# Performance work log

Hardware: AMD Instinct MI355X
Metric: run time of the kernel (lower is better)

Reference implementation:

```python
import jax, jax.numpy as jnp
import numpy as np

T_STEPS = 10          # hardcoded T_pos = T_neg = 10 in the source
SCALE = 0.125         # hardcoded attention scale
N_HEADS, N_KV_HEADS, HEAD_DIM = 32, 8, 128
DIM, HIDDEN = 4096, 14336
EPS = 1e-5

def _spike(x):
    # IFNode Heaviside fire (forward only; spikes are exact 0/1)
    return (x >= 0.0).astype(x.dtype)

def if_node(x_seq):
    """spikingjelly IFNode, step_mode='m': v += x; fire at v>=1; hard reset to 0."""
    def step(v, xt):
        v = v + xt
        s = _spike(v - 1.0)
        v = v * (1.0 - s)
        return v, s
    _, spikes = jax.lax.scan(step, jnp.zeros_like(x_seq[0]), x_seq)
    return spikes  # [T, ...]

def if_proj(x2d, W):
    # linear proj of constant-over-time input, then IF spiking over T steps
    y = x2d @ W.T                                   # [N, dout]
    return if_node(jnp.broadcast_to(y[None], (T_STEPS,) + y.shape))  # [T, N, dout]

def rmsnorm(x, w):
    return x * jax.lax.rsqrt(jnp.mean(x * x, axis=-1, keepdims=True) + EPS) * w

def attention(x, wq, wk, wv, wo):
    N, C = x.shape
    xp, xn = jax.nn.relu(x), jax.nn.relu(-x)
    xq = if_proj(xp, wq) - if_proj(xn, wq)          # [T, N, H*D]
    xk = if_proj(xp, wk) - if_proj(xn, wk)          # [T, N, Hkv*D]
    xv = if_proj(xp, wv) - if_proj(xn, wv)
    rep = N_HEADS // N_KV_HEADS
    xq = xq.reshape(T_STEPS, N, N_HEADS, HEAD_DIM)
    # repeat_interleave along token dim + view == tile over kv-head axis
    xk = jnp.tile(xk.reshape(T_STEPS, N, N_KV_HEADS, HEAD_DIM), (1, 1, rep, 1))
    xv = jnp.tile(xv.reshape(T_STEPS, N, N_KV_HEADS, HEAD_DIM), (1, 1, rep, 1))
    # NOTE: source computes per-token head-mixing scores [T,N,H,H], not token attention
    attn = jnp.einsum('tnid,tnjd->tnij', xq, xk) * SCALE
    xa = jnp.einsum('tnij,tnjd->tnid', attn, xv)    # [T,N,H,D]
    xa = jnp.swapaxes(xa, -1, -2).reshape(T_STEPS, N, C)  # transpose(-1,-2).reshape
    return (xa @ wo.T).mean(0)

def ffn(x, w1, w2, w3):
    xp, xn = jax.nn.relu(x), jax.nn.relu(-x)
    x_w3 = if_proj(xp, w3) - if_proj(xn, w3)        # [T, N, hidden]
    x_w1p = if_proj(xp, w1)                          # only positive branch for w1
    return (x_w1p.mean(0) * x_w3.mean(0)) @ w2.T

def setup_inputs() -> dict:
    ks = jax.random.split(jax.random.key(0), 9)
    std = 0.02
    return {
        'x': jax.random.normal(ks[0], (256, DIM), jnp.float32),
        'freqs_cis': jnp.zeros((256, HEAD_DIM // 2), jnp.float32),
        'attn_norm_w': jnp.ones((DIM,), jnp.float32),
        'ffn_norm_w': jnp.ones((DIM,), jnp.float32),
        'wq': std * jax.random.normal(ks[1], (N_HEADS * HEAD_DIM, DIM), jnp.float32),
        'wk': std * jax.random.normal(ks[2], (N_KV_HEADS * HEAD_DIM, DIM), jnp.float32),
        'wv': std * jax.random.normal(ks[3], (N_KV_HEADS * HEAD_DIM, DIM), jnp.float32),
        'wo': std * jax.random.normal(ks[4], (DIM, N_HEADS * HEAD_DIM), jnp.float32),
        'w1': std * jax.random.normal(ks[5], (HIDDEN, DIM), jnp.float32),
        'w2': std * jax.random.normal(ks[6], (DIM, HIDDEN), jnp.float32),
        'w3': std * jax.random.normal(ks[7], (HIDDEN, DIM), jnp.float32),
    }

def reference(x, freqs_cis, attn_norm_w, ffn_norm_w, wq, wk, wv, wo, w1, w2, w3):
    h = x + attention(rmsnorm(x, attn_norm_w), wq, wk, wv, wo)
    out = h + ffn(rmsnorm(h, ffn_norm_w), w1, w2, w3)
    return out
```

## Files before the change

### kernel.cpp

```cpp
#include <hip/hip_runtime.h>
#include <math.h>


typedef double f64x4 __attribute__((ext_vector_type(4)));

__device__ __forceinline__ unsigned spike_pat_d(double y) {
    double v = 0.0; unsigned p = 0u;
#pragma unroll
    for (int t = 0; t < 10; ++t) {
        v += y;
        bool s = (v >= 1.0);
        p |= s ? (1u << t) : 0u;
        v = s ? 0.0 : v;
    }
    return p;
}

__device__ __forceinline__ int spike_count_d(double y) {
    double v = 0.0; int c = 0;
#pragma unroll
    for (int t = 0; t < 10; ++t) {
        v += y;
        bool s = (v >= 1.0);
        c += s ? 1 : 0;
        v = s ? 0.0 : v;
    }
    return c;
}

__global__ __launch_bounds__(256) void rms_f_kernel(const float* __restrict__ x,
                                                    const float* __restrict__ w,
                                                    double* __restrict__ out)
{
    const int row = blockIdx.x, tid = threadIdx.x;
    const float4* xr = (const float4*)(x + (size_t)row * 4096);
    const float4* wr = (const float4*)w;
    double* orow = out + (size_t)row * 4096;
    float4 v[4];
    double ss = 0.0;
#pragma unroll
    for (int i = 0; i < 4; ++i) {
        v[i] = xr[tid + (i << 8)];
        ss += (double)v[i].x * v[i].x + (double)v[i].y * v[i].y +
              (double)v[i].z * v[i].z + (double)v[i].w * v[i].w;
    }
#pragma unroll
    for (int off = 32; off > 0; off >>= 1) ss += __shfl_down(ss, off, 64);
    __shared__ double red[4];
    if ((tid & 63) == 0) red[tid >> 6] = ss;
    __syncthreads();
    double m = (red[0] + red[1] + red[2] + red[3]) * (1.0 / 4096.0);
    double sc = 1.0 / sqrt(m + 1e-5);
#pragma unroll
    for (int i = 0; i < 4; ++i) {
        float4 wv = wr[tid + (i << 8)];
        int b = (tid + (i << 8)) << 2;
        orow[b + 0] = ((double)v[i].x * sc) * (double)wv.x;
        orow[b + 1] = ((double)v[i].y * sc) * (double)wv.y;
        orow[b + 2] = ((double)v[i].z * sc) * (double)wv.z;
        orow[b + 3] = ((double)v[i].w * sc) * (double)wv.w;
    }
}

__global__ __launch_bounds__(256) void rms_d_kernel(const double* __restrict__ x,
                                                    const float* __restrict__ w,
                                                    double* __restrict__ out)
{
    const int row = blockIdx.x, tid = threadIdx.x;
    const double2* xr = (const double2*)(x + (size_t)row * 4096);
    const float2* wr = (const float2*)w;
    double* orow = out + (size_t)row * 4096;
    double2 v[8];
    double ss = 0.0;
#pragma unroll
    for (int i = 0; i < 8; ++i) {
        v[i] = xr[tid + (i << 8)];
        ss += v[i].x * v[i].x + v[i].y * v[i].y;
    }
#pragma unroll
    for (int off = 32; off > 0; off >>= 1) ss += __shfl_down(ss, off, 64);
    __shared__ double red[4];
    if ((tid & 63) == 0) red[tid >> 6] = ss;
    __syncthreads();
    double m = (red[0] + red[1] + red[2] + red[3]) * (1.0 / 4096.0);
    double sc = 1.0 / sqrt(m + 1e-5);
#pragma unroll
    for (int i = 0; i < 8; ++i) {
        float2 wv = wr[tid + (i << 8)];
        int b = (tid + (i << 8)) << 1;
        orow[b + 0] = (v[i].x * sc) * (double)wv.x;
        orow[b + 1] = (v[i].y * sc) * (double)wv.y;
    }
}

template <int MODE, int WT>
__global__ __launch_bounds__(256, 2) void gemm_kernel(
    const void* __restrict__ Av, const void* __restrict__ A2v,
    const float* __restrict__ W, const void* __restrict__ ADDv,
    void* __restrict__ C0v, int K, int N)
{
    constexpr bool DUAL = (MODE == 0 || MODE == 1);
    constexpr int NB = DUAL ? 2 : 1;
    constexpr int BMN = 32 * WT;
    constexpr int EPT = 2 * WT;
    __shared__ __align__(16) double As[NB][16][BMN + 4];
    __shared__ __align__(16) float  Ws[16][BMN + 8];

    const int tid = threadIdx.x;
    const int m0 = blockIdx.y * BMN, n0 = blockIdx.x * BMN;

    const int lrow = tid / (16 / EPT);
    const int lk   = (tid % (16 / EPT)) * EPT;

    const int l  = tid & 63;
    const int wid = tid >> 6;
    const int wm = wid >> 1, wn = wid & 1;
    const int lr = l & 15;
    const int kf = l >> 4;

    f64x4 accp[WT][WT] = {};
    f64x4 accn[WT][WT] = {};

    const float* Wpt = W + (size_t)(n0 + lrow) * K + lk;
    const double* Apt = nullptr;
    const unsigned char* S1t = nullptr;
    const signed char* S3t = nullptr;
    if constexpr (MODE <= 3) {
        Apt = (const double*)Av + (size_t)(m0 + lrow) * K + lk;
    } else {
        S1t = (const unsigned char*)Av + (size_t)(m0 + lrow) * K + lk;
        S3t = (const signed char*)A2v + (size_t)(m0 + lrow) * K + lk;
    }

    auto LOAD = [&](int k0, double* a, float* w) {
        if constexpr (MODE == 4) {
            uchar4 c1 = *(const uchar4*)(S1t + k0);
            char4  c3 = *(const char4*)(S3t + k0);
            a[0] = ((double)c1.x * 0.1) * ((double)c3.x * 0.1);
            a[1] = ((double)c1.y * 0.1) * ((double)c3.y * 0.1);
            a[2] = ((double)c1.z * 0.1) * ((double)c3.z * 0.1);
            a[3] = ((double)c1.w * 0.1) * ((double)c3.w * 0.1);
        } else if constexpr (EPT == 4) {
            double2 a01 = *(const double2*)(Apt + k0);
            double2 a23 = *(const double2*)(Apt + k0 + 2);
            a[0] = a01.x; a[1] = a01.y; a[2] = a23.x; a[3] = a23.y;
        } else {
            double2 a01 = *(const double2*)(Apt + k0);
            a[0] = a01.x; a[1] = a01.y;
        }
        if constexpr (EPT == 4) {
            float4 wv = *(const float4*)(Wpt + k0);
            w[0] = wv.x; w[1] = wv.y; w[2] = wv.z; w[3] = wv.w;
        } else {
            float2 wv = *(const float2*)(Wpt + k0);
            w[0] = wv.x; w[1] = wv.y;
        }
    };

    double a_cur[EPT]; float w_cur[EPT];
    LOAD(0, a_cur, w_cur);

    for (int k0 = 0; k0 < K; k0 += 16) {
#pragma unroll
        for (int j = 0; j < EPT; ++j) {
            if constexpr (DUAL) {
                As[0][lk + j][lrow] = fmax(a_cur[j], 0.0);
                As[1][lk + j][lrow] = fmax(-a_cur[j], 0.0);
            } else if constexpr (MODE == 2) {
                As[0][lk + j][lrow] = fmax(a_cur[j], 0.0);
            } else {
                As[0][lk + j][lrow] = a_cur[j];
            }
            Ws[lk + j][lrow] = w_cur[j];
        }
        __syncthreads();

        double a_nxt[EPT]; float w_nxt[EPT];
        if (k0 + 16 < K) LOAD(k0 + 16, a_nxt, w_nxt);

#pragma unroll
        for (int ks = 0; ks < 4; ++ks) {
            const int kk = (ks << 2) + kf;
            double b[WT], p[WT];
#pragma unroll
            for (int nt = 0; nt < WT; ++nt)
                b[nt] = (double)Ws[kk][wn * (16 * WT) + nt * 16 + lr];
#pragma unroll
            for (int mt = 0; mt < WT; ++mt)
                p[mt] = As[0][kk][wm * (16 * WT) + mt * 16 + lr];
#pragma unroll
            for (int mt = 0; mt < WT; ++mt)
#pragma unroll
                for (int nt = 0; nt < WT; ++nt)
                    accp[mt][nt] = __builtin_amdgcn_mfma_f64_16x16x4f64(
                        p[mt], b[nt], accp[mt][nt], 0, 0, 0);
            if constexpr (DUAL) {
                double q[WT];
#pragma unroll
                for (int mt = 0; mt < WT; ++mt)
                    q[mt] = As[1][kk][wm * (16 * WT) + mt * 16 + lr];
#pragma unroll
                for (int mt = 0; mt < WT; ++mt)
#pragma unroll
                    for (int nt = 0; nt < WT; ++nt)
                        accn[mt][nt] = __builtin_amdgcn_mfma_f64_16x16x4f64(
                            q[mt], b[nt], accn[mt][nt], 0, 0, 0);
            }
        }
        __syncthreads();

#pragma unroll
        for (int j = 0; j < EPT; ++j) a_cur[j] = a_nxt[j];
#pragma unroll
        for (int j = 0; j < EPT; ++j) w_cur[j] = w_nxt[j];
    }

#pragma unroll
    for (int mt = 0; mt < WT; ++mt) {
#pragma unroll
        for (int nt = 0; nt < WT; ++nt) {
#pragma unroll
            for (int r = 0; r < 4; ++r) {
                const int m = m0 + wm * (16 * WT) + mt * 16 + (kf << 2) + r;
                const int n = n0 + wn * (16 * WT) + nt * 16 + lr;
                const size_t idx = (size_t)m * N + n;
                const double vp = accp[mt][nt][r];
                if constexpr (MODE == 0) {
                    const double vn = accn[mt][nt][r];
                    ((unsigned*)C0v)[idx] =
                        spike_pat_d(vp) | (spike_pat_d(vn) << 16);
                } else if constexpr (MODE == 1) {
                    const double vn = accn[mt][nt][r];
                    ((signed char*)C0v)[idx] =
                        (signed char)(spike_count_d(vp) - spike_count_d(vn));
                } else if constexpr (MODE == 2) {
                    ((unsigned char*)C0v)[idx] =
                        (unsigned char)spike_count_d(vp);
                } else if constexpr (MODE == 3) {
                    ((double*)C0v)[idx] =
                        (double)((const float*)ADDv)[idx] + vp;
                } else {
                    ((float*)C0v)[idx] =
                        (float)(((const double*)ADDv)[idx] + vp);
                }
            }
        }
    }
}

__global__ __launch_bounds__(256) void attn_kernel(
    const unsigned* __restrict__ patq_g, const unsigned* __restrict__ patk_g,
    const unsigned* __restrict__ patv_g, double* __restrict__ Aout)
{
    __shared__ __align__(16) unsigned patq[4096];
    __shared__ __align__(16) unsigned patk[1024];
    __shared__ __align__(16) unsigned patv[1024];
    __shared__ int S8[10][32][8];
    const int n = blockIdx.x, tid = threadIdx.x;

    const uint4* q4 = (const uint4*)(patq_g + (size_t)n * 4096);
#pragma unroll
    for (int r = 0; r < 4; ++r)
        ((uint4*)patq)[tid + (r << 8)] = q4[tid + (r << 8)];
    ((uint4*)patk)[tid] = ((const uint4*)(patk_g + (size_t)n * 1024))[tid];
    ((uint4*)patv)[tid] = ((const uint4*)(patv_g + (size_t)n * 1024))[tid];
    __syncthreads();

    const int hi = tid >> 3;
    const int j8 = tid & 7;

    int sacc[10] = {0, 0, 0, 0, 0, 0, 0, 0, 0, 0};
    for (int d = 0; d < 128; ++d) {
        unsigned q = patq[(hi << 7) + d];
        unsigned k = patk[(j8 << 7) + d];
        unsigned qp = q & 0xFFFFu, qn = q >> 16;
        unsigned kp = k & 0xFFFFu, kn = k >> 16;
        unsigned pos = (qp & kp) | (qn & kn);
        unsigned neg = (qp & kn) | (qn & kp);
#pragma unroll
        for (int t = 0; t < 10; ++t)
            sacc[t] += (int)((pos >> t) & 1u) - (int)((neg >> t) & 1u);
    }
#pragma unroll
    for (int t = 0; t < 10; ++t) S8[t][hi][j8] = sacc[t];
    __syncthreads();

    float xacc[16];
#pragma unroll
    for (int dd = 0; dd < 16; ++dd) xacc[dd] = 0.f;

    for (int t = 0; t < 10; ++t) {
        int s8r[8];
#pragma unroll
        for (int jj = 0; jj < 8; ++jj) s8r[jj] = S8[t][hi][jj];
#pragma unroll
        for (int dd = 0; dd < 16; ++dd) {
            int d = (j8 << 4) + dd;
            int acc = 0;
#pragma unroll
            for (int jj = 0; jj < 8; ++jj) {
                unsigned v = patv[(jj << 7) + d];
                int vv = (int)((v >> t) & 1u) - (int)((v >> (t + 16)) & 1u);
                acc += s8r[jj] * vv;
            }
            xacc[dd] += 0.5f * (float)acc;
        }
    }
#pragma unroll
    for (int dd = 0; dd < 16; ++dd) {
        int d = (j8 << 4) + dd;
        Aout[(size_t)n * 4096 + (d << 5) + hi] = (double)xacc[dd] / 10.0;
    }
}

extern "C" void kernel_launch(void* const* d_in, const int* in_sizes, int n_in,
                              void* d_out, int out_size, void* d_ws, size_t ws_size,
                              hipStream_t stream)
{
    const float* x   = (const float*)d_in[0];
    const float* anw = (const float*)d_in[2];
    const float* fnw = (const float*)d_in[3];
    const float* wq  = (const float*)d_in[4];
    const float* wk  = (const float*)d_in[5];
    const float* wv  = (const float*)d_in[6];
    const float* wo  = (const float*)d_in[7];
    const float* w1  = (const float*)d_in[8];
    const float* w2  = (const float*)d_in[9];
    const float* w3  = (const float*)d_in[10];
    float* out = (float*)d_out;

    double* h1 = (double*)d_ws;
    double* Ap = h1 + 1048576;
    double* hb = Ap + 1048576;
    double* h2 = hb + 1048576;
    unsigned* patq = (unsigned*)(h2 + 1048576);
    unsigned* patk = patq + 1048576;
    unsigned* patv = patk + 262144;
    unsigned char* s1 = (unsigned char*)(patv + 262144);
    signed char*  s3 = (signed char*)(s1 + 3670016);

    dim3 blk(256);
    rms_f_kernel<<<dim3(256), blk, 0, stream>>>(x, anw, h1);
    gemm_kernel<0, 2><<<dim3(64, 4), blk, 0, stream>>>(h1, nullptr, wq, nullptr, patq, 4096, 4096);
    gemm_kernel<0, 1><<<dim3(32, 8), blk, 0, stream>>>(h1, nullptr, wk, nullptr, patk, 4096, 1024);
    gemm_kernel<0, 1><<<dim3(32, 8), blk, 0, stream>>>(h1, nullptr, wv, nullptr, patv, 4096, 1024);
    attn_kernel<<<dim3(256), blk, 0, stream>>>(patq, patk, patv, Ap);
    gemm_kernel<3, 2><<<dim3(64, 4), blk, 0, stream>>>(Ap, nullptr, wo, x, hb, 4096, 4096);
    rms_d_kernel<<<dim3(256), blk, 0, stream>>>(hb, fnw, h2);
    gemm_kernel<1, 2><<<dim3(224, 4), blk, 0, stream>>>(h2, nullptr, w3, nullptr, s3, 4096, 14336);
    gemm_kernel<2, 2><<<dim3(224, 4), blk, 0, stream>>>(h2, nullptr, w1, nullptr, s1, 4096, 14336);
    gemm_kernel<4, 2><<<dim3(64, 4), blk, 0, stream>>>(s1, s3, w2, hb, out, 14336, 4096);
}
```

Baseline: 4.347 ms.

## Double-buffer GEMM shared tiles, fuse QKV and FFN13 launches, derive negative branch algebraically

The GEMM body now keeps two shared-memory buffers, so the next K-slice is stored while the current one is consumed, leaving one barrier per iteration instead of two. The dual relu(x)/relu(-x) path stores the raw activation once, applies fmax when reading it, and recovers the negative product as relu(x)·W − x·W. This removes the second As buffer and its extra stores. The Q/K/V GEMMs become one launch, as do the w3/w1 FFN GEMMs, which cuts launch count and fills the GPU better. The risk is that the subtraction changes f64 rounding slightly, which could flip spike thresholds right at the boundary.

After: 3.910 ms. -10.1%, faster.

```diff
diff --git a/kernel.cpp b/kernel.cpp
--- a/kernel.cpp
+++ b/kernel.cpp
@@ -93,33 +93,27 @@
     }
 }
 
-template <int MODE, int WT>
-__global__ __launch_bounds__(256, 2) void gemm_kernel(
+template <int MODE>
+__device__ __forceinline__ void gemm_body(
     const void* __restrict__ Av, const void* __restrict__ A2v,
     const float* __restrict__ W, const void* __restrict__ ADDv,
-    void* __restrict__ C0v, int K, int N)
+    void* __restrict__ C0v, int K, int N, int m0, int n0,
+    double As[2][16][68], float Ws[2][16][72])
 {
     constexpr bool DUAL = (MODE == 0 || MODE == 1);
-    constexpr int NB = DUAL ? 2 : 1;
-    constexpr int BMN = 32 * WT;
-    constexpr int EPT = 2 * WT;
-    __shared__ __align__(16) double As[NB][16][BMN + 4];
-    __shared__ __align__(16) float  Ws[16][BMN + 8];
-
     const int tid = threadIdx.x;
-    const int m0 = blockIdx.y * BMN, n0 = blockIdx.x * BMN;
-
-    const int lrow = tid / (16 / EPT);
-    const int lk   = (tid % (16 / EPT)) * EPT;
-
-    const int l  = tid & 63;
+
+    const int lrow = tid >> 2;
+    const int lk   = (tid & 3) << 2;
+
+    const int l   = tid & 63;
     const int wid = tid >> 6;
     const int wm = wid >> 1, wn = wid & 1;
     const int lr = l & 15;
     const int kf = l >> 4;
 
-    f64x4 accp[WT][WT] = {};
-    f64x4 accn[WT][WT] = {};
+    f64x4 accA[2][2] = {};
+    f64x4 accR[2][2] = {};
 
     const float* Wpt = W + (size_t)(n0 + lrow) * K + lk;
     const double* Apt = nullptr;
@@ -140,112 +134,145 @@
             a[1] = ((double)c1.y * 0.1) * ((double)c3.y * 0.1);
             a[2] = ((double)c1.z * 0.1) * ((double)c3.z * 0.1);
             a[3] = ((double)c1.w * 0.1) * ((double)c3.w * 0.1);
-        } else if constexpr (EPT == 4) {
+        } else {
             double2 a01 = *(const double2*)(Apt + k0);
             double2 a23 = *(const double2*)(Apt + k0 + 2);
             a[0] = a01.x; a[1] = a01.y; a[2] = a23.x; a[3] = a23.y;
-        } else {
-            double2 a01 = *(const double2*)(Apt + k0);
-            a[0] = a01.x; a[1] = a01.y;
-        }
-        if constexpr (EPT == 4) {
-            float4 wv = *(const float4*)(Wpt + k0);
-            w[0] = wv.x; w[1] = wv.y; w[2] = wv.z; w[3] = wv.w;
-        } else {
-            float2 wv = *(const float2*)(Wpt + k0);
-            w[0] = wv.x; w[1] = wv.y;
-        }
+        }
+        float4 wv = *(const float4*)(Wpt + k0);
+        w[0] = wv.x; w[1] = wv.y; w[2] = wv.z; w[3] = wv.w;
     };
 
-    double a_cur[EPT]; float w_cur[EPT];
+    auto STORE = [&](int buf, const double* a, const float* w) {
+#pragma unroll
+        for (int j = 0; j < 4; ++j) {
+            if constexpr (MODE == 2)
+                As[buf][lk + j][lrow] = fmax(a[j], 0.0);
+            else
+                As[buf][lk + j][lrow] = a[j];
+            Ws[buf][lk + j][lrow] = w[j];
+        }
+    };
+
+    double a_cur[4]; float w_cur[4];
     LOAD(0, a_cur, w_cur);
-
+    STORE(0, a_cur, w_cur);
+    __syncthreads();
+
+    int p = 0;
     for (int k0 = 0; k0 < K; k0 += 16) {
-#pragma unroll
-        for (int j = 0; j < EPT; ++j) {
-            if constexpr (DUAL) {
-                As[0][lk + j][lrow] = fmax(a_cur[j], 0.0);
-                As[1][lk + j][lrow] = fmax(-a_cur[j], 0.0);
-            } else if constexpr (MODE == 2) {
-                As[0][lk + j][lrow] = fmax(a_cur[j], 0.0);
-            } else {
-                As[0][lk + j][lrow] = a_cur[j];
-            }
-            Ws[lk + j][lrow] = w_cur[j];
-        }
-        __syncthreads();
-
-        double a_nxt[EPT]; float w_nxt[EPT];
-        if (k0 + 16 < K) LOAD(k0 + 16, a_nxt, w_nxt);
+        const bool last = (k0 + 16 >= K);
+        double a_nxt[4]; float w_nxt[4];
+        if (!last) LOAD(k0 + 16, a_nxt, w_nxt);
 
 #pragma unroll
         for (int ks = 0; ks < 4; ++ks) {
             const int kk = (ks << 2) + kf;
-            double b[WT], p[WT];
-#pragma unroll
-            for (int nt = 0; nt < WT; ++nt)
-                b[nt] = (double)Ws[kk][wn * (16 * WT) + nt * 16 + lr];
-#pragma unroll
-            for (int mt = 0; mt < WT; ++mt)
-                p[mt] = As[0][kk][wm * (16 * WT) + mt * 16 + lr];
-#pragma unroll
-            for (int mt = 0; mt < WT; ++mt)
-#pragma unroll
-                for (int nt = 0; nt < WT; ++nt)
-                    accp[mt][nt] = __builtin_amdgcn_mfma_f64_16x16x4f64(
-                        p[mt], b[nt], accp[mt][nt], 0, 0, 0);
+            double b0 = (double)Ws[p][kk][wn * 32 + lr];
+            double b1 = (double)Ws[p][kk][wn * 32 + 16 + lr];
+            double r0 = As[p][kk][wm * 32 + lr];
+            double r1 = As[p][kk][wm * 32 + 16 + lr];
             if constexpr (DUAL) {
-                double q[WT];
-#pragma unroll
-                for (int mt = 0; mt < WT; ++mt)
-                    q[mt] = As[1][kk][wm * (16 * WT) + mt * 16 + lr];
-#pragma unroll
-                for (int mt = 0; mt < WT; ++mt)
-#pragma unroll
-                    for (int nt = 0; nt < WT; ++nt)
-                        accn[mt][nt] = __builtin_amdgcn_mfma_f64_16x16x4f64(
-                            q[mt], b[nt], accn[mt][nt], 0, 0, 0);
+                double q0 = fmax(r0, 0.0), q1 = fmax(r1, 0.0);
+                accA[0][0] = __builtin_amdgcn_mfma_f64_16x16x4f64(q0, b0, accA[0][0], 0, 0, 0);
+                accA[0][1] = __builtin_amdgcn_mfma_f64_16x16x4f64(q0, b1, accA[0][1], 0, 0, 0);
+                accA[1][0] = __builtin_amdgcn_mfma_f64_16x16x4f64(q1, b0, accA[1][0], 0, 0, 0);
+                accA[1][1] = __builtin_amdgcn_mfma_f64_16x16x4f64(q1, b1, accA[1][1], 0, 0, 0);
+                accR[0][0] = __builtin_amdgcn_mfma_f64_16x16x4f64(r0, b0, accR[0][0], 0, 0, 0);
+                accR[0][1] = __builtin_amdgcn_mfma_f64_16x16x4f64(r0, b1, accR[0][1], 0, 0, 0);
+                accR[1][0] = __builtin_amdgcn_mfma_f64_16x16x4f64(r1, b0, accR[1][0], 0, 0, 0);
+                accR[1][1] = __builtin_amdgcn_mfma_f64_16x16x4f64(r1, b1, accR[1][1], 0, 0, 0);
+            } else {
+                accA[0][0] = __builtin_amdgcn_mfma_f64_16x16x4f64(r0, b0, accA[0][0], 0, 0, 0);
+                accA[0][1] = __builtin_amdgcn_mfma_f64_16x16x4f64(r0, b1, accA[0][1], 0, 0, 0);
+                accA[1][0] = __builtin_amdgcn_mfma_f64_16x16x4f64(r1, b0, accA[1][0], 0, 0, 0);
+                accA[1][1] = __builtin_amdgcn_mfma_f64_16x16x4f64(r1, b1, accA[1][1], 0, 0, 0);
             }
         }
-        __syncthreads();
-
-#pragma unroll
-        for (int j = 0; j < EPT; ++j) a_cur[j] = a_nxt[j];
-#pragma unroll
-        for (int j = 0; j < EPT; ++j) w_cur[j] = w_nxt[j];
-    }
-
-#pragma unroll
-    for (int mt = 0; mt < WT; ++mt) {
-#pragma unroll
-        for (int nt = 0; nt < WT; ++nt) {
+
+        if (!last) {
+            STORE(p ^ 1, a_nxt, w_nxt);
+            __syncthreads();
+            p ^= 1;
+        }
+    }
+
+#pragma unroll
+    for (int mt = 0; mt < 2; ++mt) {
+#pragma unroll
+        for (int nt = 0; nt < 2; ++nt) {
 #pragma unroll
             for (int r = 0; r < 4; ++r) {
-                const int m = m0 + wm * (16 * WT) + mt * 16 + (kf << 2) + r;
-                const int n = n0 + wn * (16 * WT) + nt * 16 + lr;
+                const int m = m0 + wm * 32 + mt * 16 + (kf << 2) + r;
+                const int n = n0 + wn * 32 + nt * 16 + lr;
                 const size_t idx = (size_t)m * N + n;
-                const double vp = accp[mt][nt][r];
+                const double vA = accA[mt][nt][r];
                 if constexpr (MODE == 0) {
-                    const double vn = accn[mt][nt][r];
+                    const double vN = vA - accR[mt][nt][r];
                     ((unsigned*)C0v)[idx] =
-                        spike_pat_d(vp) | (spike_pat_d(vn) << 16);
+                        spike_pat_d(vA) | (spike_pat_d(vN) << 16);
                 } else if constexpr (MODE == 1) {
-                    const double vn = accn[mt][nt][r];
+                    const double vN = vA - accR[mt][nt][r];
                     ((signed char*)C0v)[idx] =
-                        (signed char)(spike_count_d(vp) - spike_count_d(vn));
+                        (signed char)(spike_count_d(vA) - spike_count_d(vN));
                 } else if constexpr (MODE == 2) {
                     ((unsigned char*)C0v)[idx] =
-                        (unsigned char)spike_count_d(vp);
+                        (unsigned char)spike_count_d(vA);
                 } else if constexpr (MODE == 3) {
                     ((double*)C0v)[idx] =
-                        (double)((const float*)ADDv)[idx] + vp;
+                        (double)((const float*)ADDv)[idx] + vA;
                 } else {
                     ((float*)C0v)[idx] =
-                        (float)(((const double*)ADDv)[idx] + vp);
+                        (float)(((const double*)ADDv)[idx] + vA);
                 }
             }
         }
     }
+}
+
+__global__ __launch_bounds__(256, 2) void gemm_qkv_kernel(
+    const double* __restrict__ h1,
+    const float* __restrict__ wq, const float* __restrict__ wk,
+    const float* __restrict__ wv,
+    unsigned* __restrict__ patq, unsigned* __restrict__ patk,
+    unsigned* __restrict__ patv)
+{
+    __shared__ __align__(16) double As[2][16][68];
+    __shared__ __align__(16) float  Ws[2][16][72];
+    const int bx = blockIdx.x, m0 = blockIdx.y << 6;
+    const float* W; unsigned* C; int N, n0;
+    if (bx < 64)      { W = wq; C = patq; N = 4096; n0 = bx << 6; }
+    else if (bx < 80) { W = wk; C = patk; N = 1024; n0 = (bx - 64) << 6; }
+    else              { W = wv; C = patv; N = 1024; n0 = (bx - 80) << 6; }
+    gemm_body<0>(h1, nullptr, W, nullptr, C, 4096, N, m0, n0, As, Ws);
+}
+
+__global__ __launch_bounds__(256, 2) void gemm_ffn13_kernel(
+    const double* __restrict__ h2,
+    const float* __restrict__ w3, const float* __restrict__ w1,
+    signed char* __restrict__ s3, unsigned char* __restrict__ s1)
+{
+    __shared__ __align__(16) double As[2][16][68];
+    __shared__ __align__(16) float  Ws[2][16][72];
+    const int n0 = blockIdx.x << 6;
+    if (blockIdx.y < 4)
+        gemm_body<1>(h2, nullptr, w3, nullptr, s3, 4096, 14336,
+                     blockIdx.y << 6, n0, As, Ws);
+    else
+        gemm_body<2>(h2, nullptr, w1, nullptr, s1, 4096, 14336,
+                     (blockIdx.y - 4) << 6, n0, As, Ws);
+}
+
+template <int MODE>
+__global__ __launch_bounds__(256, 2) void gemm_kernel(
+    const void* __restrict__ Av, const void* __restrict__ A2v,
+    const float* __restrict__ W, const void* __restrict__ ADDv,
+    void* __restrict__ C0v, int K, int N)
+{
+    __shared__ __align__(16) double As[2][16][68];
+    __shared__ __align__(16) float  Ws[2][16][72];
+    gemm_body<MODE>(Av, A2v, W, ADDv, C0v, K, N,
+                    blockIdx.y << 6, blockIdx.x << 6, As, Ws);
 }
 
 __global__ __launch_bounds__(256) void attn_kernel(
@@ -341,13 +368,10 @@
 
     dim3 blk(256);
     rms_f_kernel<<<dim3(256), blk, 0, stream>>>(x, anw, h1);
-    gemm_kernel<0, 2><<<dim3(64, 4), blk, 0, stream>>>(h1, nullptr, wq, nullptr, patq, 4096, 4096);
-    gemm_kernel<0, 1><<<dim3(32, 8), blk, 0, stream>>>(h1, nullptr, wk, nullptr, patk, 4096, 1024);
-    gemm_kernel<0, 1><<<dim3(32, 8), blk, 0, stream>>>(h1, nullptr, wv, nullptr, patv, 4096, 1024);
+    gemm_qkv_kernel<<<dim3(96, 4), blk, 0, stream>>>(h1, wq, wk, wv, patq, patk, patv);
     attn_kernel<<<dim3(256), blk, 0, stream>>>(patq, patk, patv, Ap);
-    gemm_kernel<3, 2><<<dim3(64, 4), blk, 0, stream>>>(Ap, nullptr, wo, x, hb, 4096, 4096);
+    gemm_kernel<3><<<dim3(64, 4), blk, 0, stream>>>(Ap, nullptr, wo, x, hb, 4096, 4096);
     rms_d_kernel<<<dim3(256), blk, 0, stream>>>(hb, fnw, h2);
-    gemm_kernel<1, 2><<<dim3(224, 4), blk, 0, stream>>>(h2, nullptr, w3, nullptr, s3, 4096, 14336);
-    gemm_kernel<2, 2><<<dim3(224, 4), blk, 0, stream>>>(h2, nullptr, w1, nullptr, s1, 4096, 14336);
-    gemm_kernel<4, 2><<<dim3(64, 4), blk, 0, stream>>>(s1, s3, w2, hb, out, 14336, 4096);
-}
+    gemm_ffn13_kernel<<<dim3(224, 8), blk, 0, stream>>>(h2, w3, w1, s3, s1);
+    gemm_kernel<4><<<dim3(64, 4), blk, 0, stream>>>(s1, s3, w2, hb, out, 14336, 4096);
+}
```
